# Kernel optimization log

Hardware: AMD Instinct MI355X
Metric: run time of the kernel (lower is better)

The kernel has to match this reference:

```python
import jax, jax.numpy as jnp
import numpy as np

# ---- db4 filters (pywt conventions: dec_lo = rec_lo[::-1], rec_hi = qmf(rec_lo)) ----
F = 8  # db4 filter length
_rec_lo = np.array([0.23037781330885523, 0.7148465705525415, 0.6308807679295904,
                    -0.027983769416983849, -0.18703481171888114, 0.030841381835986965,
                    0.032883011666982945, -0.010597401784997278], dtype=np.float32)
_rec_hi = _rec_lo[::-1].copy()
_rec_hi[1::2] *= -1.0
REC_LO = jnp.asarray(_rec_lo)
REC_HI = jnp.asarray(_rec_hi)

MAX_LEVEL = 9  # pywt.dwt_max_level(4096, 8)


def _conv1d(x, kernel, stride=1, padding='VALID', lhs_dilation=None):
    # x: [B, L] -> correlation (XLA conv does NOT flip the kernel)
    out = jax.lax.conv_general_dilated(
        x[:, None, :], kernel[None, None, :],
        window_strides=(stride,), padding=padding,
        lhs_dilation=lhs_dilation,
        dimension_numbers=('NCH', 'OIH', 'NCH'))
    return out[:, 0, :]


def dwt(x):
    # pywt.dwt(x, 'db4', mode='symmetric'):
    # cA = np.convolve(sym_ext(x, F-1), dec_lo, 'valid')[1::2]
    # convolution with dec filter == correlation with rec filter (its reverse)
    ext = jnp.pad(x, ((0, 0), (F - 1, F - 1)), mode='symmetric')[:, 1:]
    return _conv1d(ext, REC_LO, stride=2), _conv1d(ext, REC_HI, stride=2)


def idwt(ca, cd):
    # pywt.idwt: zero-upsample coeffs, full convolution with rec filters, trim edges
    n = ca.shape[1]
    pad = ((F - 1, F - 1),)
    out = (_conv1d(ca, REC_LO[::-1], padding=pad, lhs_dilation=(2,)) +
           _conv1d(cd, REC_HI[::-1], padding=pad, lhs_dilation=(2,)))
    return out[:, F - 2:2 * n]  # output length = 2n - F + 2


def wavelet_features(x1):
    # Faithful to WaveletDWTLayer stack + WaveletParsingLayer: at each level k>=2,
    # reconstruct with details of levels k and k-1 only (others zeroed), with
    # pywt.waverec's trim-by-one rule; concatenate the 8 full-length reconstructions.
    a = x1
    cds, recs = [], []
    for level in range(1, MAX_LEVEL + 1):
        a, d = dwt(a)
        if level >= 2:
            r = idwt(jnp.zeros_like(d), d)
            for j in range(level - 2, -1, -1):
                dj = cds[j] if j == level - 2 else jnp.zeros_like(cds[j])
                if r.shape[1] == dj.shape[1] + 1:  # waverec trim rule
                    r = r[:, :-1]
                r = idwt(r, dj)
            recs.append(r)  # [B, signal_length]
        cds.append(d)
    return jnp.concatenate(recs, axis=1)  # [B, signal_length*(MAX_LEVEL-1)]


def reference(x1, x2, x3, W0, b0, W1, b1, W2, b2):
    # x2/x3 are placeholders in the original module (overwritten by layers 1/2)
    h = wavelet_features(x1)
    for W, b in ((W0, b0), (W1, b1), (W2, b2)):
        h = jax.nn.relu(h) @ W.T + b
    return h


def setup_inputs() -> dict:
    key = jax.random.key(0)
    ks = jax.random.split(key, 4)
    B, N = 2048, 4096
    D_IN, H1, H2, OUT = 32768, 181, 13, 10
    return {
        'x1': jax.random.normal(ks[0], (B, N), jnp.float32),
        'x2': jnp.zeros((B, 1, 8), jnp.float32),
        'x3': jnp.zeros((B, 1, 8), jnp.float32),
        'W0': jax.random.normal(ks[1], (H1, D_IN), jnp.float32) / np.float32(np.sqrt(D_IN)),
        'b0': jnp.zeros((H1,), jnp.float32),
        'W1': jax.random.normal(ks[2], (H2, H1), jnp.float32) / np.float32(np.sqrt(H1)),
        'b1': jnp.zeros((H2,), jnp.float32),
        'W2': jax.random.normal(ks[3], (OUT, H2), jnp.float32) / np.float32(np.sqrt(H2)),
        'b2': jnp.zeros((OUT,), jnp.float32),
    }
```

## Files before the change

kernel.cpp:

```cpp
#include <hip/hip_runtime.h>
#include <hip/hip_bf16.h>


typedef _Float16 f16x8 __attribute__((ext_vector_type(8)));
typedef _Float16 f16x4v __attribute__((ext_vector_type(4)));
typedef float f32x4 __attribute__((ext_vector_type(4)));

#define WV_THREADS 256
#define DROW 4144

#define L0 0.23037781330885523f
#define L1 0.7148465705525415f
#define L2f 0.6308807679295904f
#define L3 -0.02798376941698385f
#define L4 -0.18703481171888114f
#define L5 0.030841381835986965f
#define L6 0.032883011666982945f
#define L7 -0.010597401784997278f

#define H0 -0.010597401784997278f
#define H1 -0.032883011666982945f
#define H2 0.030841381835986965f
#define H3 0.18703481171888114f
#define H4 -0.02798376941698385f
#define H5 -0.6308807679295904f
#define H6 0.7148465705525415f
#define H7 -0.23037781330885523f

__device__ __forceinline__ int ext_idx(int j, int n) {
  return (j < 6) ? (5 - j) : ((j < n + 6) ? (j - 6) : (2 * n + 5 - j));
}

__device__ __forceinline__ void dwt2(const float* a, float* anext, float* d,
                                     int n, int m, bool store_a) {
  const int ng = (m + 1) >> 1;
  for (int g = threadIdx.x; g < ng; g += WV_THREADS) {
    float w[10];
    if (g >= 2 && 4 * g + 9 <= n + 5) {
      const float2* af = (const float2*)a + (2 * g - 3);
      float2 b0 = af[0], b1 = af[1], b2 = af[2], b3 = af[3], b4 = af[4];
      w[0] = b0.x; w[1] = b0.y; w[2] = b1.x; w[3] = b1.y; w[4] = b2.x;
      w[5] = b2.y; w[6] = b3.x; w[7] = b3.y; w[8] = b4.x; w[9] = b4.y;
    } else {
#pragma unroll
      for (int q = 0; q < 10; ++q) {
        int j = 4 * g + q;
        int jm = n + 12;
        if (j > jm) j = jm;
        w[q] = a[ext_idx(j, n)];
      }
    }
    float sl0 = w[0]*L0 + w[1]*L1 + w[2]*L2f + w[3]*L3 + w[4]*L4 + w[5]*L5 + w[6]*L6 + w[7]*L7;
    float sh0 = w[0]*H0 + w[1]*H1 + w[2]*H2  + w[3]*H3 + w[4]*H4 + w[5]*H5 + w[6]*H6 + w[7]*H7;
    float sl1 = w[2]*L0 + w[3]*L1 + w[4]*L2f + w[5]*L3 + w[6]*L4 + w[7]*L5 + w[8]*L6 + w[9]*L7;
    float sh1 = w[2]*H0 + w[3]*H1 + w[4]*H2  + w[5]*H3 + w[6]*H4 + w[7]*H5 + w[8]*H6 + w[9]*H7;
    if (2 * g + 1 < m) {
      if (store_a) *(float2*)(anext + 2 * g) = make_float2(sl0, sl1);
      *(float2*)(d + 2 * g) = make_float2(sh0, sh1);
    } else {
      if (store_a) anext[2 * g] = sl0;
      d[2 * g] = sh0;
    }
  }
}

template <bool HAS_CA, bool HAS_CD, bool FINAL>
__device__ __forceinline__ void idwt2(const float* ca, const float* cd,
                                      float* outl, _Float16* outg, int dlen) {
  const int npair = dlen - 3;
  const int ng = (npair + 1) >> 1;
  for (int g = threadIdx.x; g < ng; g += WV_THREADS) {
    float e0 = 0.f, o0 = 0.f, e1 = 0.f, o1 = 0.f;
    if (HAS_CA) {
      const float2* f = (const float2*)ca + g;
      float2 a0 = f[0], a1 = f[1], a2 = f[2];
      e0 = a1.y*L0 + a1.x*L2f + a0.y*L4 + a0.x*L6;
      o0 = a1.y*L1 + a1.x*L3  + a0.y*L5 + a0.x*L7;
      e1 = a2.x*L0 + a1.y*L2f + a1.x*L4 + a0.y*L6;
      o1 = a2.x*L1 + a1.y*L3  + a1.x*L5 + a0.y*L7;
    }
    if (HAS_CD) {
      const float2* f = (const float2*)cd + g;
      float2 d0 = f[0], d1 = f[1], d2 = f[2];
      e0 += d1.y*H0 + d1.x*H2 + d0.y*H4 + d0.x*H6;
      o0 += d1.y*H1 + d1.x*H3 + d0.y*H5 + d0.x*H7;
      e1 += d2.x*H0 + d1.y*H2 + d1.x*H4 + d0.y*H6;
      o1 += d2.x*H1 + d1.y*H3 + d1.x*H5 + d0.y*H7;
    }
    bool full = (2 * g + 1 < npair);
    if (FINAL) {
      if (full) {
        f16x4v h;
        h[0] = (_Float16)fmaxf(e0, 0.f); h[1] = (_Float16)fmaxf(o0, 0.f);
        h[2] = (_Float16)fmaxf(e1, 0.f); h[3] = (_Float16)fmaxf(o1, 0.f);
        *(f16x4v*)(outg + 4 * g) = h;
      } else {
        outg[4 * g]     = (_Float16)fmaxf(e0, 0.f);
        outg[4 * g + 1] = (_Float16)fmaxf(o0, 0.f);
      }
    } else {
      if (full) *(float4*)(outl + 4 * g) = make_float4(e0, o0, e1, o1);
      else      *(float2*)(outl + 4 * g) = make_float2(e0, o0);
    }
  }
}

__global__ __launch_bounds__(WV_THREADS) void wv_analysis_cvt(
    const float* __restrict__ x, float* __restrict__ dG,
    const float* __restrict__ W0, _Float16* __restrict__ Bw) {
  __shared__ float r1[4104];
  __shared__ float r2[2056];
  const int tid = threadIdx.x;

  if (blockIdx.x >= 2048) {
    size_t i = ((size_t)(blockIdx.x - 2048) * 256 + tid) * 4;
    int rowc = (int)(i >> 15);
    f16x4v h;
    if (rowc < 181) {
      const float4 v = *(const float4*)(W0 + i);
      h[0] = (_Float16)v.x; h[1] = (_Float16)v.y;
      h[2] = (_Float16)v.z; h[3] = (_Float16)v.w;
    } else {
      h[0] = (_Float16)0.f; h[1] = (_Float16)0.f;
      h[2] = (_Float16)0.f; h[3] = (_Float16)0.f;
    }
    *(f16x4v*)(Bw + i) = h;
    return;
  }

  const int NLa[10]  = {4096, 2051, 1029, 518, 262, 134, 70, 38, 22, 14};
  const int DOFF[10] = {0, 0, 2052, 3082, 3600, 3862, 3996, 4066, 4104, 4126};
  const int LOFF[10] = {0, 0, 1036, 520, 2068, 1040, 2332, 1176, 2404, 1216};
  const int row = blockIdx.x;

  const float4* xr = (const float4*)(x + (size_t)row * 4096);
  for (int i = tid; i < 1024; i += WV_THREADS) ((float4*)r1)[i] = xr[i];
  __syncthreads();

  float* dr = dG + (size_t)row * DROW;
  dwt2(r1, r2, dr + DOFF[1], NLa[0], NLa[1], true);
  __syncthreads();
  const float* ap = r2;
  float* an = r1;
  for (int lev = 2; lev <= 9; ++lev) {
    float* dbuf = ((lev & 1) ? r2 : r1) + LOFF[lev];
    dwt2(ap, an, dbuf, NLa[lev - 1], NLa[lev], lev < 9);
    __syncthreads();
    const float* t = ap; ap = an; an = (float*)t;
  }
  for (int lev = 2; lev <= 9; ++lev) {
    const float* src = ((lev & 1) ? r2 : r1) + LOFF[lev];
    float* dst = dr + DOFF[lev];
    for (int i = tid; i < NLa[lev]; i += WV_THREADS) dst[i] = src[i];
  }
}

__global__ __launch_bounds__(WV_THREADS, 6) void wv_synth(
    const float* __restrict__ dG, _Float16* __restrict__ A) {
  __shared__ float s1[2052];
  __shared__ float s2[2052];
  const int NLa[10]  = {4096, 2051, 1029, 518, 262, 134, 70, 38, 22, 14};
  const int DOFF[10] = {0, 0, 2052, 3082, 3600, 3862, 3996, 4066, 4104, 4126};
  const int row = blockIdx.x;
  const int L = 2 + blockIdx.y;
  const int tid = threadIdx.x;
  const float* dr = dG + (size_t)row * DROW;

  float* cur = s1;
  float* nxt = s2;
  int startj = L - 2;
  if (L >= 6) {
    if (tid < 64) {
      idwt2<false, true, false>(nullptr, dr + DOFF[L], cur, nullptr, NLa[L]);
      asm volatile("s_waitcnt lgkmcnt(0)" ::: "memory");
      for (int j = L - 2; j >= 5; --j) {
        if (j == L - 2)
          idwt2<true, true, false>(cur, dr + DOFF[j + 1], nxt, nullptr, NLa[j + 1]);
        else
          idwt2<true, false, false>(cur, nullptr, nxt, nullptr, NLa[j + 1]);
        asm volatile("s_waitcnt lgkmcnt(0)" ::: "memory");
        float* t = cur; cur = nxt; nxt = t;
      }
    } else {
      for (int j = L - 2; j >= 5; --j) { float* t = cur; cur = nxt; nxt = t; }
    }
    __syncthreads();
    startj = 4;
  } else {
    idwt2<false, true, false>(nullptr, dr + DOFF[L], cur, nullptr, NLa[L]);
    __syncthreads();
  }
  for (int j = startj; j >= 1; --j) {
    if (j == L - 2)
      idwt2<true, true, false>(cur, dr + DOFF[j + 1], nxt, nullptr, NLa[j + 1]);
    else
      idwt2<true, false, false>(cur, nullptr, nxt, nullptr, NLa[j + 1]);
    __syncthreads();
    float* t = cur; cur = nxt; nxt = t;
  }
  _Float16* og = A + (size_t)row * 32768 + (size_t)(L - 2) * 4096;
  if (L == 2)
    idwt2<true, true, true>(cur, dr + DOFF[1], nullptr, og, 2051);
  else
    idwt2<true, false, true>(cur, nullptr, nullptr, og, 2051);
}

__device__ __forceinline__ void load_lds16(const void* g, void* l) {
  __builtin_amdgcn_global_load_lds((__attribute__((address_space(1))) unsigned int*)g,
                                   (__attribute__((address_space(3))) unsigned int*)l,
                                   16, 0, 0);
}

__global__ __launch_bounds__(256, 2) void gemm_kernel(
    const _Float16* __restrict__ A, const _Float16* __restrict__ Bw,
    float* __restrict__ P, int kchunk) {
  __shared__ _Float16 As[128 * 64];
  __shared__ _Float16 Bs[192 * 64];
  const int tid = threadIdx.x;
  const int lane = tid & 63;
  const int wave = tid >> 6;
  const int m0 = blockIdx.x * 128;
  const int k0 = blockIdx.y * kchunk;
  const int nstages = kchunk >> 6;

  f32x4 acc[2][12];
#pragma unroll
  for (int mt = 0; mt < 2; ++mt)
#pragma unroll
    for (int nt = 0; nt < 12; ++nt) acc[mt][nt] = (f32x4){0.f, 0.f, 0.f, 0.f};

  for (int ks = 0; ks < nstages; ++ks) {
    const int kbase = k0 + (ks << 6);
    __syncthreads();
#pragma unroll
    for (int t = 0; t < 4; ++t) {
      int g = ((wave * 4 + t) << 6) + lane;
      int r = g >> 3, cs = g & 7;
      const _Float16* gp = A + (size_t)(m0 + r) * 32768 + kbase + ((cs ^ (r & 7)) << 3);
      load_lds16(gp, (char*)As + (size_t)((wave * 4 + t) << 10));
    }
#pragma unroll
    for (int t = 0; t < 6; ++t) {
      int g = ((wave * 6 + t) << 6) + lane;
      int r = g >> 3, cs = g & 7;
      const _Float16* gp = Bw + (size_t)r * 32768 + kbase + ((cs ^ (r & 7)) << 3);
      load_lds16(gp, (char*)Bs + (size_t)((wave * 6 + t) << 10));
    }
    __syncthreads();
#pragma unroll
    for (int kk = 0; kk < 2; ++kk) {
      const int chunk = kk * 4 + (lane >> 4);
      f16x8 af[2];
#pragma unroll
      for (int mt = 0; mt < 2; ++mt) {
        int r = wave * 32 + mt * 16 + (lane & 15);
        af[mt] = *(const f16x8*)(As + r * 64 + ((chunk ^ (r & 7)) << 3));
      }
#pragma unroll
      for (int nt = 0; nt < 12; ++nt) {
        int rb = nt * 16 + (lane & 15);
        f16x8 bf = *(const f16x8*)(Bs + rb * 64 + ((chunk ^ (rb & 7)) << 3));
        acc[0][nt] = __builtin_amdgcn_mfma_f32_16x16x32_f16(af[0], bf, acc[0][nt], 0, 0, 0);
        acc[1][nt] = __builtin_amdgcn_mfma_f32_16x16x32_f16(af[1], bf, acc[1][nt], 0, 0, 0);
      }
    }
  }
  float* Pp = P + ((size_t)blockIdx.y * 2048 + m0) * 192;
#pragma unroll
  for (int mt = 0; mt < 2; ++mt)
#pragma unroll
    for (int nt = 0; nt < 12; ++nt)
#pragma unroll
      for (int r4 = 0; r4 < 4; ++r4) {
        int rr = wave * 32 + mt * 16 + ((lane >> 4) << 2) + r4;
        int cc = nt * 16 + (lane & 15);
        Pp[(size_t)rr * 192 + cc] = acc[mt][nt][r4];
      }
}

__global__ __launch_bounds__(256) void mlp_kernel(
    const float* __restrict__ P, const float* __restrict__ b0,
    const float* __restrict__ W1, const float* __restrict__ b1,
    const float* __restrict__ W2, const float* __restrict__ b2,
    float* __restrict__ out, int nsplit) {
  __shared__ float part[4][193];
  __shared__ float h1[192];
  __shared__ float h2[13];
  const int row = blockIdx.x;
  const int t = threadIdx.x;
  const int g = t >> 6;
  const int l = t & 63;

  float a0 = 0.f, a1 = 0.f, a2 = 0.f;
  const int per = nsplit >> 2;
  for (int si = 0; si < per; ++si) {
    int s = g + (si << 2);
    const float* Pr = P + ((size_t)s * 2048 + row) * 192;
    a0 += Pr[l]; a1 += Pr[64 + l]; a2 += Pr[128 + l];
  }
  part[g][l] = a0; part[g][64 + l] = a1; part[g][128 + l] = a2;
  __syncthreads();

  if (t < 192) {
    float v = part[0][t] + part[1][t] + part[2][t] + part[3][t];
    h1[t] = (t < 181) ? fmaxf(v + b0[t], 0.f) : 0.f;
  }
  __syncthreads();

#pragma unroll
  for (int r = 0; r < 4; ++r) {
    int j = g + (r << 2);
    if (j < 13) {
      float v = 0.f;
#pragma unroll
      for (int q = 0; q < 3; ++q) {
        int n = l + (q << 6);
        if (n < 181) v += h1[n] * W1[j * 181 + n];
      }
      for (int off = 32; off >= 1; off >>= 1) v += __shfl_down(v, off);
      if (l == 0) h2[j] = fmaxf(v + b1[j], 0.f);
    }
  }
  __syncthreads();

  if (t < 10) {
    float c = b2[t];
#pragma unroll
    for (int j = 0; j < 13; ++j) c += h2[j] * W2[t * 13 + j];
    out[(size_t)row * 10 + t] = c;
  }
}

extern "C" void kernel_launch(void* const* d_in, const int* in_sizes, int n_in,
                              void* d_out, int out_size, void* d_ws, size_t ws_size,
                              hipStream_t stream) {
  const float* x1 = (const float*)d_in[0];
  const float* W0 = (const float*)d_in[3];
  const float* b0 = (const float*)d_in[4];
  const float* W1 = (const float*)d_in[5];
  const float* b1 = (const float*)d_in[6];
  const float* W2 = (const float*)d_in[7];
  const float* b2 = (const float*)d_in[8];
  float* out = (float*)d_out;

  char* ws = (char*)d_ws;
  const size_t A_BYTES = (size_t)2048 * 32768 * 2;
  const size_t B_BYTES = (size_t)192 * 32768 * 2;
  _Float16* Afeat = (_Float16*)ws;
  _Float16* Bw = (_Float16*)(ws + A_BYTES);
  float* Dq = (float*)(ws + A_BYTES + B_BYTES);
  float* P = (float*)(ws + A_BYTES + B_BYTES);

  int nsplit = 32;
  while (nsplit > 1 &&
         A_BYTES + B_BYTES + (size_t)nsplit * 2048 * 192 * 4 > ws_size)
    nsplit >>= 1;

  wv_analysis_cvt<<<2048 + 6144, WV_THREADS, 0, stream>>>(x1, Dq, W0, Bw);
  dim3 sg(2048, 8);
  wv_synth<<<sg, WV_THREADS, 0, stream>>>(Dq, Afeat);
  dim3 gg(16, nsplit);
  gemm_kernel<<<gg, 256, 0, stream>>>(Afeat, Bw, P, 32768 / nsplit);
  mlp_kernel<<<2048, 256, 0, stream>>>(P, b0, W1, b1, W2, b2, out, nsplit);
}
```

Before: 228.2 us.

## Widen final idwt to 8 outputs per thread and drop single-wave deep-level path

The final reconstruction stage gets a dedicated routine in which each thread computes 8 outputs and writes them as one 16-byte fp16 store, replacing 4 outputs with a boundary branch. The special path where only the first wave handled levels 6+ without block barriers is removed, so all levels now use the full block with __syncthreads between stages. This makes the final store wider and the code simpler, at the cost of extra barriers and idle threads on the small deep levels.

Measured after the change: 229.9 us. Within noise of the previous version (+0.7%).

```diff
diff --git a/kernel.cpp b/kernel.cpp
--- a/kernel.cpp
+++ b/kernel.cpp
@@ -64,9 +64,9 @@
   }
 }
 
-template <bool HAS_CA, bool HAS_CD, bool FINAL>
+template <bool HAS_CA, bool HAS_CD>
 __device__ __forceinline__ void idwt2(const float* ca, const float* cd,
-                                      float* outl, _Float16* outg, int dlen) {
+                                      float* outl, int dlen) {
   const int npair = dlen - 3;
   const int ng = (npair + 1) >> 1;
   for (int g = threadIdx.x; g < ng; g += WV_THREADS) {
@@ -88,20 +88,47 @@
       o1 += d2.x*H1 + d1.y*H3 + d1.x*H5 + d0.y*H7;
     }
     bool full = (2 * g + 1 < npair);
-    if (FINAL) {
-      if (full) {
-        f16x4v h;
-        h[0] = (_Float16)fmaxf(e0, 0.f); h[1] = (_Float16)fmaxf(o0, 0.f);
-        h[2] = (_Float16)fmaxf(e1, 0.f); h[3] = (_Float16)fmaxf(o1, 0.f);
-        *(f16x4v*)(outg + 4 * g) = h;
-      } else {
-        outg[4 * g]     = (_Float16)fmaxf(e0, 0.f);
-        outg[4 * g + 1] = (_Float16)fmaxf(o0, 0.f);
-      }
-    } else {
-      if (full) *(float4*)(outl + 4 * g) = make_float4(e0, o0, e1, o1);
-      else      *(float2*)(outl + 4 * g) = make_float2(e0, o0);
-    }
+    if (full) *(float4*)(outl + 4 * g) = make_float4(e0, o0, e1, o1);
+    else      *(float2*)(outl + 4 * g) = make_float2(e0, o0);
+  }
+}
+
+template <bool HAS_CD>
+__device__ __forceinline__ void idwt_final4(const float* ca, const float* cd,
+                                            _Float16* outg) {
+  for (int g = threadIdx.x; g < 512; g += WV_THREADS) {
+    const float2* f = (const float2*)ca + 2 * g;
+    float2 a0 = f[0], a1 = f[1], a2 = f[2], a3 = f[3];
+    float c0 = a0.x, c1 = a0.y, c2 = a1.x, c3 = a1.y,
+          c4 = a2.x, c5 = a2.y, c6 = a3.x;
+    float e0 = c3*L0 + c2*L2f + c1*L4 + c0*L6;
+    float o0 = c3*L1 + c2*L3  + c1*L5 + c0*L7;
+    float e1 = c4*L0 + c3*L2f + c2*L4 + c1*L6;
+    float o1 = c4*L1 + c3*L3  + c2*L5 + c1*L7;
+    float e2 = c5*L0 + c4*L2f + c3*L4 + c2*L6;
+    float o2 = c5*L1 + c4*L3  + c3*L5 + c2*L7;
+    float e3 = c6*L0 + c5*L2f + c4*L4 + c3*L6;
+    float o3 = c6*L1 + c5*L3  + c4*L5 + c3*L7;
+    if (HAS_CD) {
+      const float2* fd = (const float2*)cd + 2 * g;
+      float2 d0 = fd[0], d1 = fd[1], d2 = fd[2], d3 = fd[3];
+      float q0 = d0.x, q1 = d0.y, q2 = d1.x, q3 = d1.y,
+            q4 = d2.x, q5 = d2.y, q6 = d3.x;
+      e0 += q3*H0 + q2*H2 + q1*H4 + q0*H6;
+      o0 += q3*H1 + q2*H3 + q1*H5 + q0*H7;
+      e1 += q4*H0 + q3*H2 + q2*H4 + q1*H6;
+      o1 += q4*H1 + q3*H3 + q2*H5 + q1*H7;
+      e2 += q5*H0 + q4*H2 + q3*H4 + q2*H6;
+      o2 += q5*H1 + q4*H3 + q3*H5 + q2*H7;
+      e3 += q6*H0 + q5*H2 + q4*H4 + q3*H6;
+      o3 += q6*H1 + q5*H3 + q4*H5 + q3*H7;
+    }
+    f16x8 h;
+    h[0] = (_Float16)fmaxf(e0, 0.f); h[1] = (_Float16)fmaxf(o0, 0.f);
+    h[2] = (_Float16)fmaxf(e1, 0.f); h[3] = (_Float16)fmaxf(o1, 0.f);
+    h[4] = (_Float16)fmaxf(e2, 0.f); h[5] = (_Float16)fmaxf(o2, 0.f);
+    h[6] = (_Float16)fmaxf(e3, 0.f); h[7] = (_Float16)fmaxf(o3, 0.f);
+    *(f16x8*)(outg + 8 * g) = h;
   }
 }
 
@@ -163,46 +190,25 @@
   const int DOFF[10] = {0, 0, 2052, 3082, 3600, 3862, 3996, 4066, 4104, 4126};
   const int row = blockIdx.x;
   const int L = 2 + blockIdx.y;
-  const int tid = threadIdx.x;
   const float* dr = dG + (size_t)row * DROW;
 
+  idwt2<false, true>(nullptr, dr + DOFF[L], s1, NLa[L]);
+  __syncthreads();
   float* cur = s1;
   float* nxt = s2;
-  int startj = L - 2;
-  if (L >= 6) {
-    if (tid < 64) {
-      idwt2<false, true, false>(nullptr, dr + DOFF[L], cur, nullptr, NLa[L]);
-      asm volatile("s_waitcnt lgkmcnt(0)" ::: "memory");
-      for (int j = L - 2; j >= 5; --j) {
-        if (j == L - 2)
-          idwt2<true, true, false>(cur, dr + DOFF[j + 1], nxt, nullptr, NLa[j + 1]);
-        else
-          idwt2<true, false, false>(cur, nullptr, nxt, nullptr, NLa[j + 1]);
-        asm volatile("s_waitcnt lgkmcnt(0)" ::: "memory");
-        float* t = cur; cur = nxt; nxt = t;
-      }
-    } else {
-      for (int j = L - 2; j >= 5; --j) { float* t = cur; cur = nxt; nxt = t; }
-    }
-    __syncthreads();
-    startj = 4;
-  } else {
-    idwt2<false, true, false>(nullptr, dr + DOFF[L], cur, nullptr, NLa[L]);
-    __syncthreads();
-  }
-  for (int j = startj; j >= 1; --j) {
+  for (int j = L - 2; j >= 1; --j) {
     if (j == L - 2)
-      idwt2<true, true, false>(cur, dr + DOFF[j + 1], nxt, nullptr, NLa[j + 1]);
+      idwt2<true, true>(cur, dr + DOFF[j + 1], nxt, NLa[j + 1]);
     else
-      idwt2<true, false, false>(cur, nullptr, nxt, nullptr, NLa[j + 1]);
+      idwt2<true, false>(cur, nullptr, nxt, NLa[j + 1]);
     __syncthreads();
     float* t = cur; cur = nxt; nxt = t;
   }
   _Float16* og = A + (size_t)row * 32768 + (size_t)(L - 2) * 4096;
   if (L == 2)
-    idwt2<true, true, true>(cur, dr + DOFF[1], nullptr, og, 2051);
+    idwt_final4<true>(cur, dr + DOFF[1], og);
   else
-    idwt2<true, false, true>(cur, nullptr, nullptr, og, 2051);
+    idwt_final4<false>(cur, nullptr, og);
 }
 
 __device__ __forceinline__ void load_lds16(const void* g, void* l) {
```
